# Kernel tuning notes

Hardware: AMD Instinct MI355X
Metric: run time of the kernel (lower is better)

Reference implementation:

```python
import jax, jax.numpy as jnp
import numpy as np

N_QUBITS = 4
N_LAYERS = 2
BATCH = 524288


def _apply_1q(state, U, wire, batched):
    """Apply a 2x2 gate U on `wire`. state: [B,2,2,2,2]; U: [B,2,2] if batched else [2,2]."""
    ax = wire + 1
    s = jnp.moveaxis(state, ax, 1)
    if batched:
        s = jnp.einsum('bij,bj...->bi...', U, s)
    else:
        s = jnp.einsum('ij,bj...->bi...', U, s)
    return jnp.moveaxis(s, 1, ax)


def _apply_cnot(state, control, target):
    cax, tax = control + 1, target + 1
    s0 = jnp.take(state, 0, axis=cax)
    s1 = jnp.take(state, 1, axis=cax)
    t_ax = tax - 1 if tax > cax else tax  # target axis after removing control axis
    s1 = jnp.flip(s1, axis=t_ax)
    return jnp.stack([s0, s1], axis=cax)


def _circuit(x, weight):
    B = x.shape[0]
    # Angle encoding: RY(tanh(x_i) * pi) per wire (per-sample angles)
    theta = jnp.tanh(x) * jnp.pi  # [B, 4]
    state = jnp.zeros((B,) + (2,) * N_QUBITS, jnp.complex64)
    state = state.at[(slice(None),) + (0,) * N_QUBITS].set(1.0)
    for q in range(N_QUBITS):
        h = theta[:, q] * 0.5
        c, s = jnp.cos(h), jnp.sin(h)
        Ury = jnp.stack([jnp.stack([c, -s], -1), jnp.stack([s, c], -1)], -2).astype(jnp.complex64)  # [B,2,2]
        state = _apply_1q(state, Ury, q, batched=True)
    for layer in range(N_LAYERS):
        for q in range(N_QUBITS):
            hy = weight[layer, q, 0] * 0.5
            cy, sy = jnp.cos(hy), jnp.sin(hy)
            Uy = jnp.stack([jnp.stack([cy, -sy]), jnp.stack([sy, cy])]).astype(jnp.complex64)
            state = _apply_1q(state, Uy, q, batched=False)
            hz = weight[layer, q, 1] * 0.5
            ez = jnp.exp(-1j * hz.astype(jnp.complex64))
            z0 = jnp.zeros((), jnp.complex64)
            Uz = jnp.stack([jnp.stack([ez, z0]), jnp.stack([z0, jnp.conj(ez)])])
            state = _apply_1q(state, Uz, q, batched=False)
        for q in range(N_QUBITS):
            state = _apply_cnot(state, q, (q + 1) % N_QUBITS)
    # <Z_i> = P(bit_i = 0) - P(bit_i = 1)
    probs = jnp.abs(state) ** 2  # [B,2,2,2,2] float32
    outs = []
    for q in range(N_QUBITS):
        other_axes = tuple(a for a in range(1, N_QUBITS + 1) if a != q + 1)
        marg = probs.sum(other_axes)  # [B,2]
        outs.append(marg[:, 0] - marg[:, 1])
    return jnp.stack(outs, axis=-1).astype(jnp.float32)  # [B,4]


def setup_inputs() -> dict:
    key = jax.random.key(0)
    kx, kw = jax.random.split(key)
    x = jax.random.normal(kx, (BATCH, N_QUBITS), dtype=jnp.float32)
    weight = jax.random.normal(kw, (N_LAYERS, N_QUBITS, 2), dtype=jnp.float32) * 0.1
    return {"x": x, "weight": weight}


def reference(x, weight):
    return _circuit(x, weight)
```

## Files before the change

kernel.cpp:

```cpp
#include <hip/hip_runtime.h>
#include <math.h>


#define HALF_PI_F 1.57079632679489661923f

__global__ __launch_bounds__(256) void build_C4(
    const float* __restrict__ weight,
    float4* __restrict__ C4g)
{
    __shared__ float cw[16], sw[16];
    __shared__ float Ur[16][16], Ui[16][16];
    __shared__ float A[4][16][16];

    const int tid = threadIdx.x;
    if (tid < 16) {
        float h = 0.5f * weight[tid];
        __sincosf(h, &sw[tid], &cw[tid]);
    }
    __syncthreads();

    if (tid < 16) {
        const int col = tid;
        float re[16], im[16];
        #pragma unroll
        for (int i = 0; i < 16; ++i) { re[i] = 0.f; im[i] = 0.f; }
        re[col] = 1.f;

        #pragma unroll
        for (int layer = 0; layer < 2; ++layer) {
            #pragma unroll
            for (int q = 0; q < 4; ++q) {
                float cy = cw[layer*8 + q*2 + 0];
                float sy = sw[layer*8 + q*2 + 0];
                float cz = cw[layer*8 + q*2 + 1];
                float sz = sw[layer*8 + q*2 + 1];
                int st = 8 >> q;
                #pragma unroll
                for (int i = 0; i < 16; ++i) {
                    if (i & st) continue;
                    int j = i | st;
                    float r0 = re[i], r1 = re[j], i0 = im[i], i1 = im[j];
                    float nr0 = cy*r0 - sy*r1;
                    float nr1 = sy*r0 + cy*r1;
                    float ni0 = cy*i0 - sy*i1;
                    float ni1 = sy*i0 + cy*i1;
                    re[i] = nr0*cz + ni0*sz;
                    im[i] = ni0*cz - nr0*sz;
                    re[j] = nr1*cz - ni1*sz;
                    im[j] = ni1*cz + nr1*sz;
                }
            }
            #pragma unroll
            for (int q = 0; q < 4; ++q) {
                int cb = 8 >> q;
                int tb = 8 >> ((q + 1) & 3);
                #pragma unroll
                for (int i = 0; i < 16; ++i) {
                    if ((i & cb) && !(i & tb)) {
                        int j = i | tb;
                        float tr = re[i]; re[i] = re[j]; re[j] = tr;
                        float ti = im[i]; im[i] = im[j]; im[j] = ti;
                    }
                }
            }
        }
        #pragma unroll
        for (int i = 0; i < 16; ++i) { Ur[i][col] = re[i]; Ui[i][col] = im[i]; }
    }
    __syncthreads();

    for (int e = tid; e < 1024; e += 256) {
        int q = e >> 8, j = (e >> 4) & 15, k = e & 15;
        float sum = 0.f;
        for (int i = 0; i < 16; ++i) {
            float t = Ur[i][j]*Ur[i][k] + Ui[i][j]*Ui[i][k];
            sum += (i & (8 >> q)) ? -t : t;
        }
        A[q][j][k] = sum;
    }
    __syncthreads();

    if (tid < 100) {
        const int pu[10] = {0,0,0,0,1,1,1,2,2,3};
        const int pv[10] = {0,1,2,3,1,2,3,2,3,3};
        int pi = tid / 10, qi = tid % 10;
        int u = pu[pi], v = pv[pi], r = pu[qi], sI = pv[qi];
        int a1s[2] = {u, v}, a2s[2] = {v, u};
        int b1s[2] = {r, sI}, b2s[2] = {sI, r};
        int na = (u == v) ? 1 : 2;
        int nb = (r == sI) ? 1 : 2;
        float acc[4] = {0.f, 0.f, 0.f, 0.f};
        for (int ia = 0; ia < na; ++ia)
            for (int ib = 0; ib < nb; ++ib) {
                int j = a1s[ia]*4 + b1s[ib];
                int k = a2s[ia]*4 + b2s[ib];
                #pragma unroll
                for (int q = 0; q < 4; ++q) acc[q] += A[q][j][k];
            }
        C4g[tid] = float4{acc[0], acc[1], acc[2], acc[3]};
    }
}

__global__ __launch_bounds__(256) void qmain(
    const float* __restrict__ x,
    const float4* __restrict__ C4g,
    float* __restrict__ out,
    int B)
{
    const int s0 = blockIdx.x * 256 + threadIdx.x;

    float4 xv = (s0 < B) ? reinterpret_cast<const float4*>(x)[s0]
                         : float4{0.f, 0.f, 0.f, 0.f};

    const int pu[10] = {0,0,0,0,1,1,1,2,2,3};
    const int pv[10] = {0,1,2,3,1,2,3,2,3,3};

    float P[10], Q[10];
    {
        float xs[4] = {xv.x, xv.y, xv.z, xv.w};
        float c[4], s[4];
        #pragma unroll
        for (int q = 0; q < 4; ++q) {
            float e = __expf(2.f * xs[q]);
            float t = 1.f - __fdividef(2.f, e + 1.f);
            __sincosf(t * HALF_PI_F, &s[q], &c[q]);
        }
        float a4[4] = {c[0]*c[1], c[0]*s[1], s[0]*c[1], s[0]*s[1]};
        float b4[4] = {c[2]*c[3], c[2]*s[3], s[2]*c[3], s[2]*s[3]};
        #pragma unroll
        for (int i2 = 0; i2 < 10; ++i2) {
            P[i2] = a4[pu[i2]] * a4[pv[i2]];
            Q[i2] = b4[pu[i2]] * b4[pv[i2]];
        }
    }

    float z0 = 0.f, z1 = 0.f, z2 = 0.f, z3 = 0.f;
    #pragma unroll
    for (int pi = 0; pi < 10; ++pi) {
        float t0 = 0.f, t1 = 0.f, t2 = 0.f, t3 = 0.f;
        #pragma unroll
        for (int qi = 0; qi < 10; ++qi) {
            float4 cv = C4g[pi*10 + qi];
            float qv = Q[qi];
            t0 = fmaf(cv.x, qv, t0);
            t1 = fmaf(cv.y, qv, t1);
            t2 = fmaf(cv.z, qv, t2);
            t3 = fmaf(cv.w, qv, t3);
        }
        float pvf = P[pi];
        z0 = fmaf(pvf, t0, z0);
        z1 = fmaf(pvf, t1, z1);
        z2 = fmaf(pvf, t2, z2);
        z3 = fmaf(pvf, t3, z3);
    }

    if (s0 < B)
        reinterpret_cast<float4*>(out)[s0] = float4{z0, z1, z2, z3};
}

extern "C" void kernel_launch(void* const* d_in, const int* in_sizes, int n_in,
                              void* d_out, int out_size, void* d_ws, size_t ws_size,
                              hipStream_t stream) {
    const float* x = (const float*)d_in[0];
    const float* w = (const float*)d_in[1];
    float* out = (float*)d_out;
    float4* C4g = (float4*)d_ws;
    int B = in_sizes[0] / 4;

    build_C4<<<1, 256, 0, stream>>>(w, C4g);
    int grid = (B + 255) / 256;
    qmain<<<grid, 256, 0, stream>>>(x, C4g, out, B);
}
```

Baseline: 72.34 us.

## Fuse coefficient build into main kernel with flag-based inter-block sync

Merges the single-block coefficient-building kernel into the main per-sample kernel, removing one launch. Block 0 builds the 100-entry coefficient table and publishes it through a release store of a per-call token. The other blocks load x and compute their encoding terms first, then spin on the flag with an acquire load before reading the table. The tanh and sincos step is also rewritten as a hardware reciprocal plus the amdgcn sin/cos builtins, which take the angle in revolutions. The spin-wait relies on block 0 being scheduled while other blocks wait, and it ties correctness to a static host-side token counter.

```diff
diff --git a/kernel.cpp b/kernel.cpp
--- a/kernel.cpp
+++ b/kernel.cpp
@@ -2,115 +2,118 @@
 #include <math.h>
 
 
-#define HALF_PI_F 1.57079632679489661923f
+__global__ __launch_bounds__(256, 8) void qfused(
+    const float* __restrict__ x,
+    const float* __restrict__ weight,
+    float* __restrict__ out,
+    float4* __restrict__ C4w,
+    const float4* __restrict__ C4r,
+    int* __restrict__ flag,
+    int token,
+    int B)
+{
+    const int tid = threadIdx.x;
+    const int s0 = blockIdx.x * 256 + tid;
 
-__global__ __launch_bounds__(256) void build_C4(
-    const float* __restrict__ weight,
-    float4* __restrict__ C4g)
-{
-    __shared__ float cw[16], sw[16];
-    __shared__ float Ur[16][16], Ui[16][16];
-    __shared__ float A[4][16][16];
+    float4 xv = (s0 < B) ? reinterpret_cast<const float4*>(x)[s0]
+                         : float4{0.f, 0.f, 0.f, 0.f};
 
-    const int tid = threadIdx.x;
-    if (tid < 16) {
-        float h = 0.5f * weight[tid];
-        __sincosf(h, &sw[tid], &cw[tid]);
-    }
-    __syncthreads();
+    if (blockIdx.x == 0) {
+        __shared__ float cw[16], sw[16];
+        __shared__ float Ur[16][16], Ui[16][16];
+        __shared__ float A[4][16][16];
 
-    if (tid < 16) {
-        const int col = tid;
-        float re[16], im[16];
-        #pragma unroll
-        for (int i = 0; i < 16; ++i) { re[i] = 0.f; im[i] = 0.f; }
-        re[col] = 1.f;
+        if (tid < 16) {
+            float h = 0.5f * weight[tid];
+            __sincosf(h, &sw[tid], &cw[tid]);
+        }
+        __syncthreads();
 
-        #pragma unroll
-        for (int layer = 0; layer < 2; ++layer) {
+        if (tid < 16) {
+            const int col = tid;
+            float re[16], im[16];
             #pragma unroll
-            for (int q = 0; q < 4; ++q) {
-                float cy = cw[layer*8 + q*2 + 0];
-                float sy = sw[layer*8 + q*2 + 0];
-                float cz = cw[layer*8 + q*2 + 1];
-                float sz = sw[layer*8 + q*2 + 1];
-                int st = 8 >> q;
+            for (int i = 0; i < 16; ++i) { re[i] = 0.f; im[i] = 0.f; }
+            re[col] = 1.f;
+
+            #pragma unroll
+            for (int layer = 0; layer < 2; ++layer) {
                 #pragma unroll
-                for (int i = 0; i < 16; ++i) {
-                    if (i & st) continue;
-                    int j = i | st;
-                    float r0 = re[i], r1 = re[j], i0 = im[i], i1 = im[j];
-                    float nr0 = cy*r0 - sy*r1;
-                    float nr1 = sy*r0 + cy*r1;
-                    float ni0 = cy*i0 - sy*i1;
-                    float ni1 = sy*i0 + cy*i1;
-                    re[i] = nr0*cz + ni0*sz;
-                    im[i] = ni0*cz - nr0*sz;
-                    re[j] = nr1*cz - ni1*sz;
-                    im[j] = ni1*cz + nr1*sz;
+                for (int q = 0; q < 4; ++q) {
+                    float cy = cw[layer*8 + q*2 + 0];
+                    float sy = sw[layer*8 + q*2 + 0];
+                    float cz = cw[layer*8 + q*2 + 1];
+                    float sz = sw[layer*8 + q*2 + 1];
+                    int st = 8 >> q;
+                    #pragma unroll
+                    for (int i = 0; i < 16; ++i) {
+                        if (i & st) continue;
+                        int j = i | st;
+                        float r0 = re[i], r1 = re[j], i0 = im[i], i1 = im[j];
+                        float nr0 = cy*r0 - sy*r1;
+                        float nr1 = sy*r0 + cy*r1;
+                        float ni0 = cy*i0 - sy*i1;
+                        float ni1 = sy*i0 + cy*i1;
+                        re[i] = nr0*cz + ni0*sz;
+                        im[i] = ni0*cz - nr0*sz;
+                        re[j] = nr1*cz - ni1*sz;
+                        im[j] = ni1*cz + nr1*sz;
+                    }
+                }
+                #pragma unroll
+                for (int q = 0; q < 4; ++q) {
+                    int cb = 8 >> q;
+                    int tb = 8 >> ((q + 1) & 3);
+                    #pragma unroll
+                    for (int i = 0; i < 16; ++i) {
+                        if ((i & cb) && !(i & tb)) {
+                            int j = i | tb;
+                            float tr = re[i]; re[i] = re[j]; re[j] = tr;
+                            float ti = im[i]; im[i] = im[j]; im[j] = ti;
+                        }
+                    }
                 }
             }
             #pragma unroll
-            for (int q = 0; q < 4; ++q) {
-                int cb = 8 >> q;
-                int tb = 8 >> ((q + 1) & 3);
-                #pragma unroll
-                for (int i = 0; i < 16; ++i) {
-                    if ((i & cb) && !(i & tb)) {
-                        int j = i | tb;
-                        float tr = re[i]; re[i] = re[j]; re[j] = tr;
-                        float ti = im[i]; im[i] = im[j]; im[j] = ti;
-                    }
+            for (int i = 0; i < 16; ++i) { Ur[i][col] = re[i]; Ui[i][col] = im[i]; }
+        }
+        __syncthreads();
+
+        for (int e = tid; e < 1024; e += 256) {
+            int q = e >> 8, j = (e >> 4) & 15, k = e & 15;
+            float sum = 0.f;
+            for (int i = 0; i < 16; ++i) {
+                float t = Ur[i][j]*Ur[i][k] + Ui[i][j]*Ui[i][k];
+                sum += (i & (8 >> q)) ? -t : t;
+            }
+            A[q][j][k] = sum;
+        }
+        __syncthreads();
+
+        if (tid < 100) {
+            const int pu[10] = {0,0,0,0,1,1,1,2,2,3};
+            const int pv[10] = {0,1,2,3,1,2,3,2,3,3};
+            int pi = tid / 10, qi = tid % 10;
+            int u = pu[pi], v = pv[pi], r = pu[qi], sI = pv[qi];
+            int a1s[2] = {u, v}, a2s[2] = {v, u};
+            int b1s[2] = {r, sI}, b2s[2] = {sI, r};
+            int na = (u == v) ? 1 : 2;
+            int nb = (r == sI) ? 1 : 2;
+            float acc[4] = {0.f, 0.f, 0.f, 0.f};
+            for (int ia = 0; ia < na; ++ia)
+                for (int ib = 0; ib < nb; ++ib) {
+                    int j = a1s[ia]*4 + b1s[ib];
+                    int k = a2s[ia]*4 + b2s[ib];
+                    #pragma unroll
+                    for (int q = 0; q < 4; ++q) acc[q] += A[q][j][k];
                 }
-            }
+            C4w[tid] = float4{acc[0], acc[1], acc[2], acc[3]};
         }
-        #pragma unroll
-        for (int i = 0; i < 16; ++i) { Ur[i][col] = re[i]; Ui[i][col] = im[i]; }
+        __threadfence();
+        __syncthreads();
+        if (tid == 0)
+            __hip_atomic_store(flag, token, __ATOMIC_RELEASE, __HIP_MEMORY_SCOPE_AGENT);
     }
-    __syncthreads();
-
-    for (int e = tid; e < 1024; e += 256) {
-        int q = e >> 8, j = (e >> 4) & 15, k = e & 15;
-        float sum = 0.f;
-        for (int i = 0; i < 16; ++i) {
-            float t = Ur[i][j]*Ur[i][k] + Ui[i][j]*Ui[i][k];
-            sum += (i & (8 >> q)) ? -t : t;
-        }
-        A[q][j][k] = sum;
-    }
-    __syncthreads();
-
-    if (tid < 100) {
-        const int pu[10] = {0,0,0,0,1,1,1,2,2,3};
-        const int pv[10] = {0,1,2,3,1,2,3,2,3,3};
-        int pi = tid / 10, qi = tid % 10;
-        int u = pu[pi], v = pv[pi], r = pu[qi], sI = pv[qi];
-        int a1s[2] = {u, v}, a2s[2] = {v, u};
-        int b1s[2] = {r, sI}, b2s[2] = {sI, r};
-        int na = (u == v) ? 1 : 2;
-        int nb = (r == sI) ? 1 : 2;
-        float acc[4] = {0.f, 0.f, 0.f, 0.f};
-        for (int ia = 0; ia < na; ++ia)
-            for (int ib = 0; ib < nb; ++ib) {
-                int j = a1s[ia]*4 + b1s[ib];
-                int k = a2s[ia]*4 + b2s[ib];
-                #pragma unroll
-                for (int q = 0; q < 4; ++q) acc[q] += A[q][j][k];
-            }
-        C4g[tid] = float4{acc[0], acc[1], acc[2], acc[3]};
-    }
-}
-
-__global__ __launch_bounds__(256) void qmain(
-    const float* __restrict__ x,
-    const float4* __restrict__ C4g,
-    float* __restrict__ out,
-    int B)
-{
-    const int s0 = blockIdx.x * 256 + threadIdx.x;
-
-    float4 xv = (s0 < B) ? reinterpret_cast<const float4*>(x)[s0]
-                         : float4{0.f, 0.f, 0.f, 0.f};
 
     const int pu[10] = {0,0,0,0,1,1,1,2,2,3};
     const int pv[10] = {0,1,2,3,1,2,3,2,3,3};
@@ -122,8 +125,10 @@
         #pragma unroll
         for (int q = 0; q < 4; ++q) {
             float e = __expf(2.f * xs[q]);
-            float t = 1.f - __fdividef(2.f, e + 1.f);
-            __sincosf(t * HALF_PI_F, &s[q], &c[q]);
+            float uu = __builtin_amdgcn_rcpf(e + 1.f);
+            float rr = 0.5f * uu;
+            c[q] = __builtin_amdgcn_sinf(rr);
+            s[q] = __builtin_amdgcn_cosf(rr);
         }
         float a4[4] = {c[0]*c[1], c[0]*s[1], s[0]*c[1], s[0]*s[1]};
         float b4[4] = {c[2]*c[3], c[2]*s[3], s[2]*c[3], s[2]*s[3]};
@@ -134,13 +139,21 @@
         }
     }
 
+    if (blockIdx.x != 0) {
+        if (tid == 0) {
+            while (__hip_atomic_load(flag, __ATOMIC_ACQUIRE, __HIP_MEMORY_SCOPE_AGENT) != token)
+                __builtin_amdgcn_s_sleep(8);
+        }
+        __syncthreads();
+    }
+
     float z0 = 0.f, z1 = 0.f, z2 = 0.f, z3 = 0.f;
     #pragma unroll
     for (int pi = 0; pi < 10; ++pi) {
         float t0 = 0.f, t1 = 0.f, t2 = 0.f, t3 = 0.f;
         #pragma unroll
         for (int qi = 0; qi < 10; ++qi) {
-            float4 cv = C4g[pi*10 + qi];
+            float4 cv = C4r[pi*10 + qi];
             float qv = Q[qi];
             t0 = fmaf(cv.x, qv, t0);
             t1 = fmaf(cv.y, qv, t1);
@@ -164,10 +177,13 @@
     const float* x = (const float*)d_in[0];
     const float* w = (const float*)d_in[1];
     float* out = (float*)d_out;
-    float4* C4g = (float4*)d_ws;
+    float4* C4 = (float4*)d_ws;
+    int* flag = (int*)((char*)d_ws + 4096);
     int B = in_sizes[0] / 4;
 
-    build_C4<<<1, 256, 0, stream>>>(w, C4g);
+    static int token = 0x51000000;
+    ++token;
+
     int grid = (B + 255) / 256;
-    qmain<<<grid, 256, 0, stream>>>(x, C4g, out, B);
+    qfused<<<grid, 256, 0, stream>>>(x, w, out, C4, (const float4*)C4, flag, token, B);
 }
```

After: 154.3 us. +113.3%, slower.
